# Optimization experiments

Hardware: AMD Instinct MI355X
Metric: run time of the kernel (lower is better)

Reference implementation:

```python
import jax, jax.numpy as jnp
import numpy as np

B, D = 64, 1024
TAU = 1.0
NEG_SLOPE = 0.01  # torch LeakyReLU default


def setup_inputs() -> dict:
    key = jax.random.key(0)
    ks = jax.random.split(key, 7)
    lim = 1.0 / np.sqrt(D)
    return {
        "x": jax.random.normal(ks[0], (B, D), dtype=jnp.float32),
        "W1": jax.random.uniform(ks[1], (D, D), jnp.float32, -lim, lim),
        "b1": jax.random.uniform(ks[2], (D,), jnp.float32, -lim, lim),
        "W2": jax.random.uniform(ks[3], (D, D), jnp.float32, -lim, lim),
        "b2": jax.random.uniform(ks[4], (D,), jnp.float32, -lim, lim),
        "W3": jax.random.uniform(ks[5], (2, D), jnp.float32, -lim, lim),
        "b3": jax.random.uniform(ks[6], (2,), jnp.float32, -lim, lim),
    }


def _leaky(h):
    return jnp.where(h >= 0, h, NEG_SLOPE * h)


def _neural_sort(scores):
    # scores: [B, D]
    d = scores.shape[1]
    s = scores[..., None]                                  # [B, D, 1]
    A = jnp.abs(s - jnp.swapaxes(s, 1, 2))                 # [B, D, D] pairwise |s_i - s_j|
    # A @ (ones @ ones^T) == row-sum of A broadcast over columns
    Bsum = jnp.sum(A, axis=-1, keepdims=True)              # [B, D, 1]
    scaling = (d - 1 - 2 * jnp.arange(d)).astype(scores.dtype)  # (d+1-2*(i+1))
    C = s * scaling[None, None, :]                         # [B, D, D]
    P_max = jnp.swapaxes(C - Bsum, 1, 2)                   # [B, D, D]
    return jax.nn.softmax(P_max / TAU, axis=-1)


def reference(x, W1, b1, W2, b2, W3, b3):
    P_hat = _neural_sort(x)                                # [B, D, D]
    xs = jnp.einsum("bij,bj->bi", P_hat, x)                # soft-sorted x
    h = _leaky(xs @ W1.T + b1)
    h = _leaky(h @ W2.T + b2)
    return h @ W3.T + b3                                   # [B, 2]
```

## Files before the change

kernel.cpp:

```cpp
#include <hip/hip_runtime.h>
#include <math.h>

constexpr int Bn = 64;
constexpr int Dn = 1024;
constexpr float LOG2E = 1.4426950408889634f;
constexpr float LN2   = 0.6931471805599453f;

__device__ __forceinline__ float exp2_fast(float v) {
#if defined(__has_builtin)
#if __has_builtin(__builtin_amdgcn_exp2f)
  return __builtin_amdgcn_exp2f(v);
#else
  return exp2f(v);
#endif
#else
  return exp2f(v);
#endif
}

__global__ __launch_bounds__(256) void k_sortsoft(
    const float* __restrict__ x, float* __restrict__ xs_out,
    float* __restrict__ out) {
  __shared__ float  xs_[Dn];
  __shared__ float2 prs_[Dn];
  __shared__ int    bkt_[Dn];
  __shared__ float4 desc_[128];
  __shared__ int   cnt[64], base_[64], off_[64];
  __shared__ float Ssum[64], cN[64], cS[64];
  __shared__ float redM[4][64], redE[4][64], redD[4][64];

  int b   = blockIdx.x >> 4;
  int rc  = blockIdx.x & 15;
  int tid = threadIdx.x;

  if (tid < 64) { cnt[tid] = 0; off_[tid] = 0; Ssum[tid] = 0.f; }
  if (blockIdx.x == 0 && tid < 128) out[tid] = 0.f;
  __syncthreads();

  float4 v4 = *(const float4*)(x + b * Dn + tid * 4);
  float xv[4] = {v4.x, v4.y, v4.z, v4.w};
  int bk[4];
#pragma unroll
  for (int u = 0; u < 4; ++u) {
    float z = exp2_fast(-2.455532f * xv[u]);
    float p = 1.f / (1.f + z);
    int t = (int)(p * 64.f);
    bk[u] = t < 0 ? 0 : (t > 63 ? 63 : t);
    atomicAdd(&cnt[bk[u]], 1);
    atomicAdd(&Ssum[bk[u]], xv[u]);
  }
  __syncthreads();

  if (tid < 64) {
    int c = cnt[tid]; int si = c;
    float fs = Ssum[tid]; float ss = fs;
#pragma unroll
    for (int d = 1; d < 64; d <<= 1) {
      int oi = __shfl_up(si, d, 64);
      float os = __shfl_up(ss, d, 64);
      if (tid >= d) { si += oi; ss += os; }
    }
    base_[tid] = si - c;
    float Stot = __shfl(ss, 63, 64);
    float Slo = ss - fs;
    cN[tid] = (float)(2 * (si - c) + c - Dn);
    cS[tid] = Stot - 2.f * Slo - fs;
  }
  __syncthreads();

#pragma unroll
  for (int u = 0; u < 4; ++u) {
    int pos = base_[bk[u]] + atomicAdd(&off_[bk[u]], 1);
    xs_[pos] = xv[u];
    bkt_[pos] = bk[u];
  }
  __syncthreads();

#pragma unroll
  for (int r = 0; r < 4; ++r) {
    int p = r * 256 + tid;
    float xp = xs_[p];
    int q = bkt_[p];
    int lo = base_[q], hi = lo + cnt[q];
    float local = 0.f;
    for (int k = lo; k < hi; ++k) local += fabsf(xp - xs_[k]);
    float Bs = fmaf(xp, cN[q], cS[q]) + local;
    prs_[p] = make_float2(xp * LOG2E, -Bs * LOG2E);
  }
  __syncthreads();

  if (tid < 128) {
    int base = tid * 8;
    float xlo = xs_[base], xhi = xlo;
    int ilo = base, ihi = base;
#pragma unroll
    for (int k = 1; k < 8; ++k) {
      float xx = xs_[base + k];
      if (xx < xlo) { xlo = xx; ilo = base + k; }
      if (xx > xhi) { xhi = xx; ihi = base + k; }
    }
    float2 plo = prs_[ilo], phi = prs_[ihi];
    desc_[tid] = make_float4(plo.x, plo.y, phi.x, phi.y);
  }
  __syncthreads();

  int w = tid >> 6, lane = tid & 63;
  int i = rc * 64 + lane;
  float sc = (float)(Dn - 1 - 2 * i);
  float gm[32];
  float m = -3.4e38f;
#pragma unroll 8
  for (int q = 0; q < 32; ++q) {
    float4 d = desc_[q * 4 + w];
    float t0 = fmaf(sc, d.x, d.y);
    float t1 = fmaf(sc, d.z, d.w);
    float g = fmaxf(t0, t1);
    gm[q] = g;
    m = fmaxf(m, g);
  }
  redM[w][lane] = m;
  __syncthreads();
  float M = fmaxf(fmaxf(redM[0][lane], redM[1][lane]),
                  fmaxf(redM[2][lane], redM[3][lane]));
  float thresh = M - 32.f;

  float se = 0.f, sd = 0.f;
#pragma unroll 4
  for (int q = 0; q < 32; ++q) {
    if (__any(gm[q] > thresh)) {
      int base = (q * 4 + w) * 8;
#pragma unroll
      for (int u = 0; u < 8; ++u) {
        float2 v = prs_[base + u];
        float e = exp2_fast(fmaf(sc, v.x, v.y - M));
        se += e;
        sd = fmaf(e, v.x, sd);
      }
    }
  }
  redE[w][lane] = se;
  redD[w][lane] = sd;
  __syncthreads();
  if (tid < 64) {
    float SE = (redE[0][lane] + redE[1][lane]) + (redE[2][lane] + redE[3][lane]);
    float SD = (redD[0][lane] + redD[1][lane]) + (redD[2][lane] + redD[3][lane]);
    xs_out[b * Dn + rc * 64 + lane] = SD / SE * LN2;
  }
}

template <bool TAIL>
__global__ __launch_bounds__(256) void layer_kernel(
    const float* __restrict__ in, const float* __restrict__ W,
    const float* __restrict__ bias, float* __restrict__ out,
    const float* __restrict__ W3, const float* __restrict__ b3,
    float* __restrict__ out2) {
  __shared__ float s[8][Dn + 4];
  __shared__ float red[8][8][16];
  __shared__ float r2[8][8][2];
  int xcd = blockIdx.x & 7;
  int idx = blockIdx.x >> 3;
  int nc = xcd * 16 + (idx & 15);
  int bc = idx >> 4;
  int tid = threadIdx.x;
  const float* src = in + bc * 8 * Dn;
#pragma unroll
  for (int u = 0; u < 8; ++u) {
    int idx2 = (u * 256 + tid) << 2;
    *(float4*)&s[idx2 >> 10][idx2 & 1023] = *(const float4*)(src + idx2);
  }
  __syncthreads();

  int bl = tid & 7;
  int nq = (tid >> 3) & 1;
  int kc = tid >> 4;
  int n0 = nc * 8 + nq * 4;
  const float* a  = &s[bl][kc * 64];
  const float* w0 = W + (size_t)(n0 + 0) * Dn + kc * 64;
  const float* w1 = W + (size_t)(n0 + 1) * Dn + kc * 64;
  const float* w2 = W + (size_t)(n0 + 2) * Dn + kc * 64;
  const float* w3 = W + (size_t)(n0 + 3) * Dn + kc * 64;
  float a0 = 0.f, a1 = 0.f, a2 = 0.f, a3 = 0.f;
#pragma unroll 4
  for (int kq = 0; kq < 16; ++kq) {
    float4 av = *(const float4*)(a + kq * 4);
    float4 b0 = *(const float4*)(w0 + kq * 4);
    float4 b1 = *(const float4*)(w1 + kq * 4);
    float4 b2 = *(const float4*)(w2 + kq * 4);
    float4 b3v = *(const float4*)(w3 + kq * 4);
    a0 = fmaf(av.x, b0.x, fmaf(av.y, b0.y, fmaf(av.z, b0.z, fmaf(av.w, b0.w, a0))));
    a1 = fmaf(av.x, b1.x, fmaf(av.y, b1.y, fmaf(av.z, b1.z, fmaf(av.w, b1.w, a1))));
    a2 = fmaf(av.x, b2.x, fmaf(av.y, b2.y, fmaf(av.z, b2.z, fmaf(av.w, b2.w, a2))));
    a3 = fmaf(av.x, b3v.x, fmaf(av.y, b3v.y, fmaf(av.z, b3v.z, fmaf(av.w, b3v.w, a3))));
  }
  red[bl][nq * 4 + 0][kc] = a0;
  red[bl][nq * 4 + 1][kc] = a1;
  red[bl][nq * 4 + 2][kc] = a2;
  red[bl][nq * 4 + 3][kc] = a3;
  __syncthreads();

  if (!TAIL) {
    if (tid < 64) {
      int bl2 = tid >> 3, nl2 = tid & 7;
      int n2 = nc * 8 + nl2;
      float hs = 0.f;
#pragma unroll
      for (int q = 0; q < 16; ++q) hs += red[bl2][nl2][q];
      float h = hs + bias[n2];
      h = h >= 0.f ? h : 0.01f * h;
      out[(bc * 8 + bl2) * Dn + n2] = h;
    }
  } else {
    if (tid < 64) {
      int bl2 = tid >> 3, nl2 = tid & 7;
      int n2 = nc * 8 + nl2;
      float hs = 0.f;
#pragma unroll
      for (int q = 0; q < 16; ++q) hs += red[bl2][nl2][q];
      float h = hs + bias[n2];
      h = h >= 0.f ? h : 0.01f * h;
      r2[bl2][nl2][0] = h * W3[n2];
      r2[bl2][nl2][1] = h * W3[Dn + n2];
    }
    __syncthreads();
    if (tid < 16) {
      int bl2 = tid >> 1, o = tid & 1;
      float t = 0.f;
#pragma unroll
      for (int q = 0; q < 8; ++q) t += r2[bl2][q][o];
      if (nc == 0) t += b3[o];
      atomicAdd(out2 + (bc * 8 + bl2) * 2 + o, t);
    }
  }
}

extern "C" void kernel_launch(void* const* d_in, const int* in_sizes, int n_in,
                              void* d_out, int out_size, void* d_ws, size_t ws_size,
                              hipStream_t stream) {
  const float* x  = (const float*)d_in[0];
  const float* W1 = (const float*)d_in[1];
  const float* b1 = (const float*)d_in[2];
  const float* W2 = (const float*)d_in[3];
  const float* b2 = (const float*)d_in[4];
  const float* W3 = (const float*)d_in[5];
  const float* b3 = (const float*)d_in[6];
  float* out = (float*)d_out;
  float* ws = (float*)d_ws;

  float* xs = ws;
  float* h1 = xs + Bn * Dn;

  k_sortsoft<<<Bn * 16, 256, 0, stream>>>(x, xs, out);
  layer_kernel<false><<<1024, 256, 0, stream>>>(xs, W1, b1, h1,
                                                nullptr, nullptr, nullptr);
  layer_kernel<true><<<1024, 256, 0, stream>>>(h1, W2, b2, nullptr,
                                               W3, b3, out);
}
```

Baseline: 109.8 us.

## Fuse sort and both MLP layers into one cooperative kernel with grid syncs

Merges the soft-sort kernel and the two linear-layer kernels into a single cooperative kernel. A shared-memory union holds each phase's buffers, and grid.sync separates the phases. The goal is to remove the launch gaps and tail drain between the three back-to-back kernels. In exchange it adds grid-wide barrier cost and imposes a 4-blocks-per-CU launch bound, which may constrain registers in the sort phase. It falls back to the three separate launches if the cooperative launch fails.

```diff
diff --git a/kernel.cpp b/kernel.cpp
--- a/kernel.cpp
+++ b/kernel.cpp
@@ -1,5 +1,8 @@
 #include <hip/hip_runtime.h>
+#include <hip/hip_cooperative_groups.h>
 #include <math.h>
+
+namespace cg = cooperative_groups;
 
 constexpr int Bn = 64;
 constexpr int Dn = 1024;
@@ -18,23 +21,34 @@
 #endif
 }
 
-__global__ __launch_bounds__(256) void k_sortsoft(
-    const float* __restrict__ x, float* __restrict__ xs_out,
-    float* __restrict__ out) {
-  __shared__ float  xs_[Dn];
-  __shared__ float2 prs_[Dn];
-  __shared__ int    bkt_[Dn];
-  __shared__ float4 desc_[128];
-  __shared__ int   cnt[64], base_[64], off_[64];
-  __shared__ float Ssum[64], cN[64], cS[64];
-  __shared__ float redM[4][64], redE[4][64], redD[4][64];
-
-  int b   = blockIdx.x >> 4;
-  int rc  = blockIdx.x & 15;
-  int tid = threadIdx.x;
-
-  if (tid < 64) { cnt[tid] = 0; off_[tid] = 0; Ssum[tid] = 0.f; }
-  if (blockIdx.x == 0 && tid < 128) out[tid] = 0.f;
+struct SortSmem {
+  float  xs_[Dn];
+  float2 prs_[Dn];
+  int    bkt_[Dn];
+  float4 desc_[128];
+  int    cnt[64], base_[64], off_[64];
+  float  Ssum[64], cN[64], cS[64];
+  float  redM[4][64], redE[4][64], redD[4][64];
+};
+struct LayerSmem {
+  float s[8][Dn + 4];
+  float red[8][8][16];
+  float r2[8][8][2];
+};
+union Smem {
+  SortSmem srt;
+  LayerSmem lyr;
+};
+
+__device__ __forceinline__ void sortsoft_phase(
+    Smem* smp, int blk, int tid, const float* __restrict__ x,
+    float* __restrict__ xs_out, float* __restrict__ out) {
+  SortSmem& sm = smp->srt;
+  int b  = blk >> 4;
+  int rc = blk & 15;
+
+  if (tid < 64) { sm.cnt[tid] = 0; sm.off_[tid] = 0; sm.Ssum[tid] = 0.f; }
+  if (blk == 0 && tid < 128) out[tid] = 0.f;
   __syncthreads();
 
   float4 v4 = *(const float4*)(x + b * Dn + tid * 4);
@@ -46,61 +60,61 @@
     float p = 1.f / (1.f + z);
     int t = (int)(p * 64.f);
     bk[u] = t < 0 ? 0 : (t > 63 ? 63 : t);
-    atomicAdd(&cnt[bk[u]], 1);
-    atomicAdd(&Ssum[bk[u]], xv[u]);
+    atomicAdd(&sm.cnt[bk[u]], 1);
+    atomicAdd(&sm.Ssum[bk[u]], xv[u]);
   }
   __syncthreads();
 
   if (tid < 64) {
-    int c = cnt[tid]; int si = c;
-    float fs = Ssum[tid]; float ss = fs;
+    int c = sm.cnt[tid]; int si = c;
+    float fs = sm.Ssum[tid]; float ss = fs;
 #pragma unroll
     for (int d = 1; d < 64; d <<= 1) {
       int oi = __shfl_up(si, d, 64);
       float os = __shfl_up(ss, d, 64);
       if (tid >= d) { si += oi; ss += os; }
     }
-    base_[tid] = si - c;
+    sm.base_[tid] = si - c;
     float Stot = __shfl(ss, 63, 64);
     float Slo = ss - fs;
-    cN[tid] = (float)(2 * (si - c) + c - Dn);
-    cS[tid] = Stot - 2.f * Slo - fs;
+    sm.cN[tid] = (float)(2 * (si - c) + c - Dn);
+    sm.cS[tid] = Stot - 2.f * Slo - fs;
   }
   __syncthreads();
 
 #pragma unroll
   for (int u = 0; u < 4; ++u) {
-    int pos = base_[bk[u]] + atomicAdd(&off_[bk[u]], 1);
-    xs_[pos] = xv[u];
-    bkt_[pos] = bk[u];
+    int pos = sm.base_[bk[u]] + atomicAdd(&sm.off_[bk[u]], 1);
+    sm.xs_[pos] = xv[u];
+    sm.bkt_[pos] = bk[u];
   }
   __syncthreads();
 
 #pragma unroll
   for (int r = 0; r < 4; ++r) {
     int p = r * 256 + tid;
-    float xp = xs_[p];
-    int q = bkt_[p];
-    int lo = base_[q], hi = lo + cnt[q];
+    float xp = sm.xs_[p];
+    int q = sm.bkt_[p];
+    int lo = sm.base_[q], hi = lo + sm.cnt[q];
     float local = 0.f;
-    for (int k = lo; k < hi; ++k) local += fabsf(xp - xs_[k]);
-    float Bs = fmaf(xp, cN[q], cS[q]) + local;
-    prs_[p] = make_float2(xp * LOG2E, -Bs * LOG2E);
+    for (int k = lo; k < hi; ++k) local += fabsf(xp - sm.xs_[k]);
+    float Bs = fmaf(xp, sm.cN[q], sm.cS[q]) + local;
+    sm.prs_[p] = make_float2(xp * LOG2E, -Bs * LOG2E);
   }
   __syncthreads();
 
   if (tid < 128) {
     int base = tid * 8;
-    float xlo = xs_[base], xhi = xlo;
+    float xlo = sm.xs_[base], xhi = xlo;
     int ilo = base, ihi = base;
 #pragma unroll
     for (int k = 1; k < 8; ++k) {
-      float xx = xs_[base + k];
+      float xx = sm.xs_[base + k];
       if (xx < xlo) { xlo = xx; ilo = base + k; }
       if (xx > xhi) { xhi = xx; ihi = base + k; }
     }
-    float2 plo = prs_[ilo], phi = prs_[ihi];
-    desc_[tid] = make_float4(plo.x, plo.y, phi.x, phi.y);
+    float2 plo = sm.prs_[ilo], phi = sm.prs_[ihi];
+    sm.desc_[tid] = make_float4(plo.x, plo.y, phi.x, phi.y);
   }
   __syncthreads();
 
@@ -111,17 +125,17 @@
   float m = -3.4e38f;
 #pragma unroll 8
   for (int q = 0; q < 32; ++q) {
-    float4 d = desc_[q * 4 + w];
+    float4 d = sm.desc_[q * 4 + w];
     float t0 = fmaf(sc, d.x, d.y);
     float t1 = fmaf(sc, d.z, d.w);
     float g = fmaxf(t0, t1);
     gm[q] = g;
     m = fmaxf(m, g);
   }
-  redM[w][lane] = m;
-  __syncthreads();
-  float M = fmaxf(fmaxf(redM[0][lane], redM[1][lane]),
-                  fmaxf(redM[2][lane], redM[3][lane]));
+  sm.redM[w][lane] = m;
+  __syncthreads();
+  float M = fmaxf(fmaxf(sm.redM[0][lane], sm.redM[1][lane]),
+                  fmaxf(sm.redM[2][lane], sm.redM[3][lane]));
   float thresh = M - 32.f;
 
   float se = 0.f, sd = 0.f;
@@ -131,37 +145,37 @@
       int base = (q * 4 + w) * 8;
 #pragma unroll
       for (int u = 0; u < 8; ++u) {
-        float2 v = prs_[base + u];
+        float2 v = sm.prs_[base + u];
         float e = exp2_fast(fmaf(sc, v.x, v.y - M));
         se += e;
         sd = fmaf(e, v.x, sd);
       }
     }
   }
-  redE[w][lane] = se;
-  redD[w][lane] = sd;
+  sm.redE[w][lane] = se;
+  sm.redD[w][lane] = sd;
   __syncthreads();
   if (tid < 64) {
-    float SE = (redE[0][lane] + redE[1][lane]) + (redE[2][lane] + redE[3][lane]);
-    float SD = (redD[0][lane] + redD[1][lane]) + (redD[2][lane] + redD[3][lane]);
+    float SE = (sm.redE[0][lane] + sm.redE[1][lane]) +
+               (sm.redE[2][lane] + sm.redE[3][lane]);
+    float SD = (sm.redD[0][lane] + sm.redD[1][lane]) +
+               (sm.redD[2][lane] + sm.redD[3][lane]);
     xs_out[b * Dn + rc * 64 + lane] = SD / SE * LN2;
   }
 }
 
-template <bool TAIL>
-__global__ __launch_bounds__(256) void layer_kernel(
-    const float* __restrict__ in, const float* __restrict__ W,
-    const float* __restrict__ bias, float* __restrict__ out,
-    const float* __restrict__ W3, const float* __restrict__ b3,
-    float* __restrict__ out2) {
-  __shared__ float s[8][Dn + 4];
-  __shared__ float red[8][8][16];
-  __shared__ float r2[8][8][2];
-  int xcd = blockIdx.x & 7;
-  int idx = blockIdx.x >> 3;
+__device__ __forceinline__ void layer_phase(
+    Smem* smp, int blk, int tid, const float* __restrict__ in,
+    const float* __restrict__ W, const float* __restrict__ bias,
+    float* __restrict__ out, bool tail, const float* __restrict__ W3,
+    const float* __restrict__ b3, float* __restrict__ out2) {
+  float (*s)[Dn + 4] = smp->lyr.s;
+  float (*red)[8][16] = smp->lyr.red;
+  float (*r2)[8][2] = smp->lyr.r2;
+  int xcd = blk & 7;
+  int idx = blk >> 3;
   int nc = xcd * 16 + (idx & 15);
   int bc = idx >> 4;
-  int tid = threadIdx.x;
   const float* src = in + bc * 8 * Dn;
 #pragma unroll
   for (int u = 0; u < 8; ++u) {
@@ -198,7 +212,7 @@
   red[bl][nq * 4 + 3][kc] = a3;
   __syncthreads();
 
-  if (!TAIL) {
+  if (!tail) {
     if (tid < 64) {
       int bl2 = tid >> 3, nl2 = tid & 7;
       int n2 = nc * 8 + nl2;
@@ -231,6 +245,43 @@
       atomicAdd(out2 + (bc * 8 + bl2) * 2 + o, t);
     }
   }
+}
+
+__global__ __launch_bounds__(256, 4) void fused_all(
+    const float* __restrict__ x,
+    const float* __restrict__ W1, const float* __restrict__ b1,
+    const float* __restrict__ W2, const float* __restrict__ b2,
+    const float* __restrict__ W3, const float* __restrict__ b3,
+    float* __restrict__ xs, float* __restrict__ h1,
+    float* __restrict__ out) {
+  __shared__ Smem sm;
+  cg::grid_group grid = cg::this_grid();
+  int blk = blockIdx.x;
+  int tid = threadIdx.x;
+
+  sortsoft_phase(&sm, blk, tid, x, xs, out);
+  grid.sync();
+  layer_phase(&sm, blk, tid, xs, W1, b1, h1, false, nullptr, nullptr, nullptr);
+  grid.sync();
+  layer_phase(&sm, blk, tid, h1, W2, b2, nullptr, true, W3, b3, out);
+}
+
+__global__ __launch_bounds__(256) void k_sortsoft(
+    const float* __restrict__ x, float* __restrict__ xs_out,
+    float* __restrict__ out) {
+  __shared__ Smem sm;
+  sortsoft_phase(&sm, blockIdx.x, threadIdx.x, x, xs_out, out);
+}
+
+template <bool TAIL>
+__global__ __launch_bounds__(256) void layer_kernel(
+    const float* __restrict__ in, const float* __restrict__ W,
+    const float* __restrict__ bias, float* __restrict__ out,
+    const float* __restrict__ W3, const float* __restrict__ b3,
+    float* __restrict__ out2) {
+  __shared__ Smem sm;
+  layer_phase(&sm, blockIdx.x, threadIdx.x, in, W, bias, out, TAIL, W3, b3,
+              out2);
 }
 
 extern "C" void kernel_launch(void* const* d_in, const int* in_sizes, int n_in,
@@ -249,9 +300,15 @@
   float* xs = ws;
   float* h1 = xs + Bn * Dn;
 
-  k_sortsoft<<<Bn * 16, 256, 0, stream>>>(x, xs, out);
-  layer_kernel<false><<<1024, 256, 0, stream>>>(xs, W1, b1, h1,
-                                                nullptr, nullptr, nullptr);
-  layer_kernel<true><<<1024, 256, 0, stream>>>(h1, W2, b2, nullptr,
-                                               W3, b3, out);
-}
+  void* args[] = {(void*)&x,  (void*)&W1, (void*)&b1, (void*)&W2, (void*)&b2,
+                  (void*)&W3, (void*)&b3, (void*)&xs, (void*)&h1, (void*)&out};
+  hipError_t e = hipLaunchCooperativeKernel(
+      (const void*)fused_all, dim3(Bn * 16), dim3(256), args, 0, stream);
+  if (e != hipSuccess) {
+    k_sortsoft<<<Bn * 16, 256, 0, stream>>>(x, xs, out);
+    layer_kernel<false><<<1024, 256, 0, stream>>>(xs, W1, b1, h1,
+                                                  nullptr, nullptr, nullptr);
+    layer_kernel<true><<<1024, 256, 0, stream>>>(h1, W2, b2, nullptr,
+                                                 W3, b3, out);
+  }
+}
```

Result: slower. 287.8 us (+162.0%).

## Use one 1024-thread block per batch row in soft-sort kernel

Applied to the files above, without the earlier changes.

The soft-sort kernel now launches one 1024-thread block per batch row instead of 16 blocks of 256 threads per row. The bucket sort and pairwise-sum preprocessing, which each of the 16 blocks used to repeat, now runs once per row. Each thread owns one output row and scans all 128 groups itself, so the cross-wave shared-memory reductions and their barriers go away. The cost is fewer blocks (64 on a GPU with many CUs) and more serial work per thread, so occupancy and latency hiding may drop.

```diff
diff --git a/kernel.cpp b/kernel.cpp
--- a/kernel.cpp
+++ b/kernel.cpp
@@ -18,7 +18,7 @@
 #endif
 }
 
-__global__ __launch_bounds__(256) void k_sortsoft(
+__global__ __launch_bounds__(1024) void k_sortsoft(
     const float* __restrict__ x, float* __restrict__ xs_out,
     float* __restrict__ out) {
   __shared__ float  xs_[Dn];
@@ -27,27 +27,23 @@
   __shared__ float4 desc_[128];
   __shared__ int   cnt[64], base_[64], off_[64];
   __shared__ float Ssum[64], cN[64], cS[64];
-  __shared__ float redM[4][64], redE[4][64], redD[4][64];
-
-  int b   = blockIdx.x >> 4;
-  int rc  = blockIdx.x & 15;
+
+  int b   = blockIdx.x;
   int tid = threadIdx.x;
 
   if (tid < 64) { cnt[tid] = 0; off_[tid] = 0; Ssum[tid] = 0.f; }
-  if (blockIdx.x == 0 && tid < 128) out[tid] = 0.f;
-  __syncthreads();
-
-  float4 v4 = *(const float4*)(x + b * Dn + tid * 4);
-  float xv[4] = {v4.x, v4.y, v4.z, v4.w};
-  int bk[4];
-#pragma unroll
-  for (int u = 0; u < 4; ++u) {
-    float z = exp2_fast(-2.455532f * xv[u]);
+  if (b == 0 && tid < 128) out[tid] = 0.f;
+  __syncthreads();
+
+  float xv = x[b * Dn + tid];
+  int bk;
+  {
+    float z = exp2_fast(-2.455532f * xv);
     float p = 1.f / (1.f + z);
     int t = (int)(p * 64.f);
-    bk[u] = t < 0 ? 0 : (t > 63 ? 63 : t);
-    atomicAdd(&cnt[bk[u]], 1);
-    atomicAdd(&Ssum[bk[u]], xv[u]);
+    bk = t < 0 ? 0 : (t > 63 ? 63 : t);
+    atomicAdd(&cnt[bk], 1);
+    atomicAdd(&Ssum[bk], xv);
   }
   __syncthreads();
 
@@ -68,24 +64,21 @@
   }
   __syncthreads();
 
-#pragma unroll
-  for (int u = 0; u < 4; ++u) {
-    int pos = base_[bk[u]] + atomicAdd(&off_[bk[u]], 1);
-    xs_[pos] = xv[u];
-    bkt_[pos] = bk[u];
-  }
-  __syncthreads();
-
-#pragma unroll
-  for (int r = 0; r < 4; ++r) {
-    int p = r * 256 + tid;
-    float xp = xs_[p];
-    int q = bkt_[p];
+  {
+    int pos = base_[bk] + atomicAdd(&off_[bk], 1);
+    xs_[pos] = xv;
+    bkt_[pos] = bk;
+  }
+  __syncthreads();
+
+  {
+    float xp = xs_[tid];
+    int q = bkt_[tid];
     int lo = base_[q], hi = lo + cnt[q];
     float local = 0.f;
     for (int k = lo; k < hi; ++k) local += fabsf(xp - xs_[k]);
     float Bs = fmaf(xp, cN[q], cS[q]) + local;
-    prs_[p] = make_float2(xp * LOG2E, -Bs * LOG2E);
+    prs_[tid] = make_float2(xp * LOG2E, -Bs * LOG2E);
   }
   __syncthreads();
 
@@ -104,48 +97,41 @@
   }
   __syncthreads();
 
-  int w = tid >> 6, lane = tid & 63;
-  int i = rc * 64 + lane;
-  float sc = (float)(Dn - 1 - 2 * i);
-  float gm[32];
-  float m = -3.4e38f;
+  float sc = (float)(Dn - 1 - 2 * tid);
+
+  float M = -3.4e38f;
 #pragma unroll 8
-  for (int q = 0; q < 32; ++q) {
-    float4 d = desc_[q * 4 + w];
+  for (int g = 0; g < 128; ++g) {
+    float4 d = desc_[g];
     float t0 = fmaf(sc, d.x, d.y);
     float t1 = fmaf(sc, d.z, d.w);
-    float g = fmaxf(t0, t1);
-    gm[q] = g;
-    m = fmaxf(m, g);
-  }
-  redM[w][lane] = m;
-  __syncthreads();
-  float M = fmaxf(fmaxf(redM[0][lane], redM[1][lane]),
-                  fmaxf(redM[2][lane], redM[3][lane]));
+    M = fmaxf(M, fmaxf(t0, t1));
+  }
   float thresh = M - 32.f;
 
-  float se = 0.f, sd = 0.f;
-#pragma unroll 4
+  float se[4] = {0.f, 0.f, 0.f, 0.f};
+  float sd[4] = {0.f, 0.f, 0.f, 0.f};
+#pragma unroll 2
   for (int q = 0; q < 32; ++q) {
-    if (__any(gm[q] > thresh)) {
-      int base = (q * 4 + w) * 8;
-#pragma unroll
-      for (int u = 0; u < 8; ++u) {
-        float2 v = prs_[base + u];
-        float e = exp2_fast(fmaf(sc, v.x, v.y - M));
-        se += e;
-        sd = fmaf(e, v.x, sd);
+#pragma unroll
+    for (int w = 0; w < 4; ++w) {
+      float4 d = desc_[q * 4 + w];
+      float gv = fmaxf(fmaf(sc, d.x, d.y), fmaf(sc, d.z, d.w));
+      if (__any(gv > thresh)) {
+        int base = (q * 4 + w) * 8;
+#pragma unroll
+        for (int u = 0; u < 8; ++u) {
+          float2 v = prs_[base + u];
+          float e = exp2_fast(fmaf(sc, v.x, v.y - M));
+          se[w] += e;
+          sd[w] = fmaf(e, v.x, sd[w]);
+        }
       }
     }
   }
-  redE[w][lane] = se;
-  redD[w][lane] = sd;
-  __syncthreads();
-  if (tid < 64) {
-    float SE = (redE[0][lane] + redE[1][lane]) + (redE[2][lane] + redE[3][lane]);
-    float SD = (redD[0][lane] + redD[1][lane]) + (redD[2][lane] + redD[3][lane]);
-    xs_out[b * Dn + rc * 64 + lane] = SD / SE * LN2;
-  }
+  float SE = (se[0] + se[1]) + (se[2] + se[3]);
+  float SD = (sd[0] + sd[1]) + (sd[2] + sd[3]);
+  xs_out[b * Dn + tid] = SD / SE * LN2;
 }
 
 template <bool TAIL>
@@ -249,7 +235,7 @@
   float* xs = ws;
   float* h1 = xs + Bn * Dn;
 
-  k_sortsoft<<<Bn * 16, 256, 0, stream>>>(x, xs, out);
+  k_sortsoft<<<Bn, 1024, 0, stream>>>(x, xs, out);
   layer_kernel<false><<<1024, 256, 0, stream>>>(xs, W1, b1, h1,
                                                 nullptr, nullptr, nullptr);
   layer_kernel<true><<<1024, 256, 0, stream>>>(h1, W2, b2, nullptr,
```

New measurement: 125.2 us. +14.0%, slower.

## Restructure GEMV layer thread mapping with swizzled LDS and shuffle reduction

Applied to the files above, without the earlier changes.

Each thread in the layer kernels now owns one output column and a 32-wide K slice for all 8 batch rows, so every weight float4 load is reused across 8 rows instead of each thread loading 4 weight rows for one batch row. The shared activation tile is XOR-swizzled to avoid bank conflicts on the new column-strided reads. The per-K-chunk partial sums are reduced with wave shuffles, leaving only a small 4-way cross-wave reduction in LDS. The aim is to cut redundant global weight traffic and LDS reduction work, at the cost of more accumulator registers and more LDS reads per thread.

```diff
diff --git a/kernel.cpp b/kernel.cpp
--- a/kernel.cpp
+++ b/kernel.cpp
@@ -154,8 +154,8 @@
     const float* __restrict__ bias, float* __restrict__ out,
     const float* __restrict__ W3, const float* __restrict__ b3,
     float* __restrict__ out2) {
-  __shared__ float s[8][Dn + 4];
-  __shared__ float red[8][8][16];
+  __shared__ float s[8 * Dn];
+  __shared__ float red2[4][8][9];
   __shared__ float r2[8][8][2];
   int xcd = blockIdx.x & 7;
   int idx = blockIdx.x >> 3;
@@ -165,46 +165,50 @@
   const float* src = in + bc * 8 * Dn;
 #pragma unroll
   for (int u = 0; u < 8; ++u) {
-    int idx2 = (u * 256 + tid) << 2;
-    *(float4*)&s[idx2 >> 10][idx2 & 1023] = *(const float4*)(src + idx2);
-  }
-  __syncthreads();
-
-  int bl = tid & 7;
-  int nq = (tid >> 3) & 1;
-  int kc = tid >> 4;
-  int n0 = nc * 8 + nq * 4;
-  const float* a  = &s[bl][kc * 64];
-  const float* w0 = W + (size_t)(n0 + 0) * Dn + kc * 64;
-  const float* w1 = W + (size_t)(n0 + 1) * Dn + kc * 64;
-  const float* w2 = W + (size_t)(n0 + 2) * Dn + kc * 64;
-  const float* w3 = W + (size_t)(n0 + 3) * Dn + kc * 64;
-  float a0 = 0.f, a1 = 0.f, a2 = 0.f, a3 = 0.f;
-#pragma unroll 4
-  for (int kq = 0; kq < 16; ++kq) {
-    float4 av = *(const float4*)(a + kq * 4);
-    float4 b0 = *(const float4*)(w0 + kq * 4);
-    float4 b1 = *(const float4*)(w1 + kq * 4);
-    float4 b2 = *(const float4*)(w2 + kq * 4);
-    float4 b3v = *(const float4*)(w3 + kq * 4);
-    a0 = fmaf(av.x, b0.x, fmaf(av.y, b0.y, fmaf(av.z, b0.z, fmaf(av.w, b0.w, a0))));
-    a1 = fmaf(av.x, b1.x, fmaf(av.y, b1.y, fmaf(av.z, b1.z, fmaf(av.w, b1.w, a1))));
-    a2 = fmaf(av.x, b2.x, fmaf(av.y, b2.y, fmaf(av.z, b2.z, fmaf(av.w, b2.w, a2))));
-    a3 = fmaf(av.x, b3v.x, fmaf(av.y, b3v.y, fmaf(av.z, b3v.z, fmaf(av.w, b3v.w, a3))));
-  }
-  red[bl][nq * 4 + 0][kc] = a0;
-  red[bl][nq * 4 + 1][kc] = a1;
-  red[bl][nq * 4 + 2][kc] = a2;
-  red[bl][nq * 4 + 3][kc] = a3;
+    int gl = u * 256 + tid;
+    int r = gl >> 8, g = gl & 255;
+    int gs = g ^ ((g >> 3) & 7);
+    *(float4*)&s[r * Dn + gs * 4] = *(const float4*)(src + gl * 4);
+  }
+  __syncthreads();
+
+  int c  = tid & 7;
+  int kc = tid >> 3;
+  int w  = tid >> 6, lane = tid & 63;
+  const float* wp = W + (size_t)(nc * 8 + c) * Dn + kc * 32;
+  float acc[8] = {0.f, 0.f, 0.f, 0.f, 0.f, 0.f, 0.f, 0.f};
+#pragma unroll
+  for (int kq = 0; kq < 8; ++kq) {
+    float4 wv = *(const float4*)(wp + kq * 4);
+    int gs = kc * 8 + (kq ^ (kc & 7));
+    const float* sp = s + gs * 4;
+#pragma unroll
+    for (int bl = 0; bl < 8; ++bl) {
+      float4 av = *(const float4*)(sp + bl * Dn);
+      acc[bl] = fmaf(av.x, wv.x, fmaf(av.y, wv.y,
+                fmaf(av.z, wv.z, fmaf(av.w, wv.w, acc[bl]))));
+    }
+  }
+#pragma unroll
+  for (int bl = 0; bl < 8; ++bl) {
+    float v = acc[bl];
+    v += __shfl_xor(v, 8, 64);
+    v += __shfl_xor(v, 16, 64);
+    v += __shfl_xor(v, 32, 64);
+    acc[bl] = v;
+  }
+  if (lane < 8) {
+#pragma unroll
+    for (int bl = 0; bl < 8; ++bl) red2[w][bl][lane] = acc[bl];
+  }
   __syncthreads();
 
   if (!TAIL) {
     if (tid < 64) {
       int bl2 = tid >> 3, nl2 = tid & 7;
       int n2 = nc * 8 + nl2;
-      float hs = 0.f;
-#pragma unroll
-      for (int q = 0; q < 16; ++q) hs += red[bl2][nl2][q];
+      float hs = (red2[0][bl2][nl2] + red2[1][bl2][nl2]) +
+                 (red2[2][bl2][nl2] + red2[3][bl2][nl2]);
       float h = hs + bias[n2];
       h = h >= 0.f ? h : 0.01f * h;
       out[(bc * 8 + bl2) * Dn + n2] = h;
@@ -213,9 +217,8 @@
     if (tid < 64) {
       int bl2 = tid >> 3, nl2 = tid & 7;
       int n2 = nc * 8 + nl2;
-      float hs = 0.f;
-#pragma unroll
-      for (int q = 0; q < 16; ++q) hs += red[bl2][nl2][q];
+      float hs = (red2[0][bl2][nl2] + red2[1][bl2][nl2]) +
+                 (red2[2][bl2][nl2] + red2[3][bl2][nl2]);
       float h = hs + bias[n2];
       h = h >= 0.f ? h : 0.01f * h;
       r2[bl2][nl2][0] = h * W3[n2];
```

Measured after the change: 104.4 us. 4.9% less time.
